# Kernel tuning notes

Measured on AMD Instinct MI355X. Metric: run time of the kernel, lower is better.

Reference implementation:

```python
import jax, jax.numpy as jnp
import numpy as np

B, T, I, H, FUT = 16384, 50, 6, 128, 30


def setup_inputs() -> dict:
    key = jax.random.key(0)
    ks = jax.random.split(key, 10)
    bound = 1.0 / np.sqrt(H)
    u = lambda k, shape: jax.random.uniform(k, shape, jnp.float32, -bound, bound)
    return {
        "history": jax.random.normal(ks[0], (B, T, I), jnp.float32),
        # GRU weights (PyTorch layout: gates stacked [r, z, n])
        "w_ih": u(ks[1], (3 * H, I)),
        "w_hh": u(ks[2], (3 * H, H)),
        "b_ih": u(ks[3], (3 * H,)),
        "b_hh": u(ks[4], (3 * H,)),
        # MLP head: Linear(H,H) -> ReLU -> Linear(H,I)
        "w1": u(ks[5], (H, H)),
        "b1": u(ks[6], (H,)),
        "w2": u(ks[7], (I, H)),
        "b2": u(ks[8], (I,)),
    }


def _gru_cell(h, x, w_ih, w_hh, b_ih, b_hh):
    # PyTorch GRU cell: gates ordered r, z, n
    gi = x @ w_ih.T + b_ih          # (B, 3H)
    gh = h @ w_hh.T + b_hh          # (B, 3H)
    i_r, i_z, i_n = jnp.split(gi, 3, axis=-1)
    h_r, h_z, h_n = jnp.split(gh, 3, axis=-1)
    r = jax.nn.sigmoid(i_r + h_r)
    z = jax.nn.sigmoid(i_z + h_z)
    n = jnp.tanh(i_n + r * h_n)
    return (1.0 - z) * n + z * h


def reference(history, w_ih, w_hh, b_ih, b_hh, w1, b1, w2, b2):
    # --- encode history: scan GRU over time ---
    h0 = jnp.zeros((history.shape[0], H), history.dtype)

    def enc_step(h, x_t):
        return _gru_cell(h, x_t, w_ih, w_hh, b_ih, b_hh), None

    h_last, _ = jax.lax.scan(enc_step, h0, jnp.swapaxes(history, 0, 1))  # (B, H)

    def head(h):
        return jax.nn.relu(h @ w1.T + b1) @ w2.T + b2  # (B, I)

    def dec_step(carry, _):
        h, x = carry
        h = _gru_cell(h, x, w_ih, w_hh, b_ih, b_hh)
        x = head(h)
        return (h, x), x

    x0 = history[:, -1]  # (B, I)
    _, preds = jax.lax.scan(dec_step, (h_last, x0), None, length=FUT)  # (FUT, B, I)
    return jnp.swapaxes(preds, 0, 1)  # (B, FUT, I)
```

## Files before the change

### kernel.cpp

```cpp
#include <hip/hip_runtime.h>

typedef _Float16 half8 __attribute__((ext_vector_type(8)));
typedef _Float16 half4 __attribute__((ext_vector_type(4)));
typedef float f32x4 __attribute__((ext_vector_type(4)));

#define ROWS 64
#define HP 136
#define HBUFSZ (ROWS * HP)
#define LOG2E 1.442695041f
#define MFMA(a,b,c) __builtin_amdgcn_mfma_f32_16x16x32_f16((a),(b),(c),0,0,0)

__global__ __launch_bounds__(512, 2)
void traj_gru(const float* __restrict__ history,
              const float* __restrict__ w_ih, const float* __restrict__ w_hh,
              const float* __restrict__ b_ih, const float* __restrict__ b_hh,
              const float* __restrict__ w1, const float* __restrict__ b1,
              const float* __restrict__ w2, const float* __restrict__ b2,
              float* __restrict__ out)
{
    __shared__ __align__(16) _Float16 hbuf[2 * HBUFSZ];
    __shared__ __align__(16) _Float16 xhist[50 * ROWS * 8];
    __shared__ __align__(16) _Float16 xdec[ROWS * 8];
    __shared__ __align__(16) _Float16 w2f[4 * 4 * 16 * 8];

    const int tid  = threadIdx.x;
    const int wave = tid >> 6;
    const int lane = tid & 63;
    const int ln16 = lane & 15;
    const int q    = lane >> 4;
    const int sw   = ln16 & 3;
    const int rowbase = blockIdx.x * ROWS;
    const int dbase = wave * 16;
    const int bblk  = wave >> 1;
    const int colin = ((wave & 1) << 4) | ln16;

    for (int i = tid; i < 2 * HBUFSZ; i += 512) hbuf[i] = (_Float16)0;
    for (int i = tid; i < ROWS * 8; i += 512) xdec[i] = (_Float16)0;
    for (int i = tid; i < 4 * 4 * 16 * 8; i += 512) w2f[i] = (_Float16)0;
    __syncthreads();
    for (int idx = tid; idx < 50 * ROWS * 8; idx += 512) {
        int c = idx & 7, tr = idx >> 3;
        int r = tr & (ROWS - 1), t = tr >> 6;
        _Float16 v;
        if (c < 6)       v = (_Float16)history[(rowbase + r) * 300 + t * 6 + c];
        else if (c == 6) v = (_Float16)1.0f;
        else             v = (_Float16)0.0f;
        xhist[idx] = v;
    }
    if (tid < ROWS) xdec[tid * 8 + 6] = (_Float16)1.0f;
    for (int idx = tid; idx < 6 * 128; idx += 512) {
        int n = idx >> 7, k = idx & 127;
        int kt = k >> 5, qq = (k >> 3) & 3, j = k & 7;
        w2f[((kt * 4 + qq) * 16 + n) * 8 + j] = (_Float16)w2[n * 128 + k];
    }

    half8 Wg[3][4];
    #pragma unroll
    for (int g = 0; g < 3; ++g) {
        float sc = (g < 2) ? -LOG2E : -2.0f * LOG2E;
        #pragma unroll
        for (int kt = 0; kt < 4; ++kt) {
            const float* p = w_hh + (g * 128 + dbase + ln16) * 128 + kt * 32 + q * 8;
            half8 v;
            #pragma unroll
            for (int j = 0; j < 8; ++j) v[j] = (_Float16)(p[j] * sc);
            Wg[g][kt] = v;
        }
    }
    half8 Wx[3];
    #pragma unroll
    for (int g = 0; g < 3; ++g) {
        float sc = (g < 2) ? -LOG2E : -2.0f * LOG2E;
        half8 v;
        #pragma unroll
        for (int j = 0; j < 8; ++j) v[j] = (_Float16)0.0f;
        if (q == 0) {
            #pragma unroll
            for (int j = 0; j < 6; ++j) v[j] = (_Float16)(w_ih[(g * 128 + dbase + ln16) * 6 + j] * sc);
        }
        Wx[g] = v;
    }
    f32x4 brr, brz, bin, bhn;
    #pragma unroll
    for (int i = 0; i < 4; ++i) {
        int d = dbase + q * 4 + i;
        brr[i] = (b_ih[d]       + b_hh[d]      ) * (-LOG2E);
        brz[i] = (b_ih[128 + d] + b_hh[128 + d]) * (-LOG2E);
        bin[i] = b_ih[256 + d] * (-2.0f * LOG2E);
        bhn[i] = b_hh[256 + d] * (-2.0f * LOG2E);
    }
    half8 Bw1[4];
    #pragma unroll
    for (int kt = 0; kt < 4; ++kt) {
        const float* p = w1 + (dbase + ln16) * 128 + kt * 32 + q * 8;
        half8 v;
        #pragma unroll
        for (int j = 0; j < 8; ++j) v[j] = (_Float16)p[j];
        Bw1[kt] = v;
    }
    const float b1r = b1[dbase + ln16];
    const float b2r = (ln16 < 6) ? b2[ln16] : 0.0f;

    float hp[4][4] = {};

    __syncthreads();

    auto gru_step = [&](int p, int t, bool enc) {
        const _Float16* hb = hbuf + p * HBUFSZ;
        _Float16*       hn = hbuf + (p ^ 1) * HBUFSZ;
        half8 Bf[2][4], Bx[2];
        f32x4 ar[2], az[2], ahh[2], an[2];

        auto loadB = [&](int c, int buf) {
            const _Float16* rp = hb + (c * 16 + ln16) * HP;
            #pragma unroll
            for (int kt = 0; kt < 4; ++kt)
                Bf[buf][kt] = *(const half8*)(rp + kt * 32 + q * 8);
            if (enc) {
                Bx[buf] = *(const half8*)(xhist + ((t * ROWS + c * 16 + ln16) << 3));
            } else {
                Bx[buf] = *(const half8*)(xdec + (c * 16 + ln16) * 8);
            }
        };
        auto mfmas = [&](int buf) {
            f32x4 r = brr, z = brz, hh = bhn, n = bin;
            __builtin_amdgcn_s_setprio(1);
            #pragma unroll
            for (int kt = 0; kt < 4; ++kt) {
                r  = MFMA(Wg[0][kt], Bf[buf][kt], r);
                z  = MFMA(Wg[1][kt], Bf[buf][kt], z);
                hh = MFMA(Wg[2][kt], Bf[buf][kt], hh);
            }
            r = MFMA(Wx[0], Bx[buf], r);
            z = MFMA(Wx[1], Bx[buf], z);
            n = MFMA(Wx[2], Bx[buf], n);
            __builtin_amdgcn_s_setprio(0);
            ar[buf] = r; az[buf] = z; ahh[buf] = hh; an[buf] = n;
        };
        auto gates = [&](int c, int cb) {
            half4 hv;
            #pragma unroll
            for (int i = 0; i < 4; ++i) {
                float r = __builtin_amdgcn_rcpf(1.0f + __builtin_amdgcn_exp2f(ar[cb][i]));
                float z = __builtin_amdgcn_rcpf(1.0f + __builtin_amdgcn_exp2f(az[cb][i]));
                float tt = an[cb][i] + r * ahh[cb][i];
                float n = 2.0f * __builtin_amdgcn_rcpf(1.0f + __builtin_amdgcn_exp2f(tt)) - 1.0f;
                float h = n + z * (hp[c][i] - n);
                hp[c][i] = h;
                hv[i] = (_Float16)h;
            }
            *(half4*)(hn + (c * 16 + ln16) * HP + dbase + q * 4) = hv;
        };

        loadB(0, 0); mfmas(0);
        #pragma unroll
        for (int c = 0; c < 4; ++c) {
            const int cb = c & 1;
            if (c < 3) { loadB(c + 1, cb ^ 1); mfmas(cb ^ 1); }
            gates(c, cb);
        }
        __syncthreads();
    };

    auto head_step = [&](int f, int p) {
        const _Float16* hb = hbuf + p * HBUFSZ;
        _Float16*       a1 = hbuf + (p ^ 1) * HBUFSZ;
        half8 Ah[2][4];
        f32x4 aa[2];
        auto loadA = [&](int c, int buf) {
            const _Float16* rp = hb + (c * 16 + ln16) * HP;
            #pragma unroll
            for (int kt = 0; kt < 4; ++kt)
                Ah[buf][kt] = *(const half8*)(rp + kt * 32 + q * 8);
        };
        auto mfh = [&](int buf) {
            f32x4 a = {0,0,0,0};
            __builtin_amdgcn_s_setprio(1);
            #pragma unroll
            for (int kt = 0; kt < 4; ++kt) a = MFMA(Ah[buf][kt], Bw1[kt], a);
            __builtin_amdgcn_s_setprio(0);
            aa[buf] = a;
        };
        auto relu4 = [&](int c, int cb) {
            #pragma unroll
            for (int i = 0; i < 4; ++i) {
                float v = aa[cb][i] + b1r;
                v = v > 0.0f ? v : 0.0f;
                a1[(c * 16 + q * 4 + i) * HP + ((bblk ^ i) << 5) + colin] = (_Float16)v;
            }
        };
        loadA(0, 0); mfh(0);
        #pragma unroll
        for (int c = 0; c < 4; ++c) {
            const int cb = c & 1;
            if (c < 3) { loadA(c + 1, cb ^ 1); mfh(cb ^ 1); }
            relu4(c, cb);
        }
        __syncthreads();
        if (wave < 4) {
            const _Float16* rp = a1 + (wave * 16 + ln16) * HP;
            f32x4 o = {0,0,0,0};
            #pragma unroll
            for (int kt = 0; kt < 4; ++kt) {
                half8 Aa = *(const half8*)(rp + ((kt ^ sw) << 5) + q * 8);
                half8 Bw = *(const half8*)&w2f[((kt * 4 + q) * 16 + ln16) * 8];
                o = MFMA(Aa, Bw, o);
            }
            if (ln16 < 6) {
                #pragma unroll
                for (int i = 0; i < 4; ++i) {
                    int row = wave * 16 + q * 4 + i;
                    float v = o[i] + b2r;
                    out[(rowbase + row) * 180 + f * 6 + ln16] = v;
                    xdec[row * 8 + ln16] = (_Float16)v;
                }
            }
        }
        __syncthreads();
    };

    int p = 0;
    #pragma unroll 1
    for (int t = 0; t < 50; ++t) { gru_step(p, t, true); p ^= 1; }
    #pragma unroll 1
    for (int f = 0; f < 30; ++f) {
        gru_step(p, f == 0 ? 49 : 0, f == 0);
        p ^= 1;
        head_step(f, p);
    }
}

extern "C" void kernel_launch(void* const* d_in, const int* in_sizes, int n_in,
                              void* d_out, int out_size, void* d_ws, size_t ws_size,
                              hipStream_t stream) {
    (void)in_sizes; (void)n_in; (void)d_ws; (void)ws_size; (void)out_size;
    traj_gru<<<dim3(16384 / ROWS), dim3(512), 0, stream>>>(
        (const float*)d_in[0], (const float*)d_in[1], (const float*)d_in[2],
        (const float*)d_in[3], (const float*)d_in[4], (const float*)d_in[5],
        (const float*)d_in[6], (const float*)d_in[7], (const float*)d_in[8],
        (float*)d_out);
}
```

Before: 288.2 us.

## Software-pipeline encoder GRU steps across time with split-half barriers

Replaces the encoder loop with a dedicated pipelined loop. The four 16-row chunks are split into two halves with a barrier between them, so the next timestep's MFMAs for the first half can run while the gate math for the second half of the current step finishes. The aim is to hide the dependency stall between the MFMA results and the transcendental gate work. It costs a second barrier per step and more live accumulator registers, which may reduce occupancy. The setprio hints are also removed from the decoder MFMA blocks.

```diff
diff --git a/kernel.cpp b/kernel.cpp
--- a/kernel.cpp
+++ b/kernel.cpp
@@ -105,6 +105,62 @@
 
     __syncthreads();
 
+    {
+        f32x4 aA[2][4], aB[2][4];
+        auto emfma = [&](int t, int c, f32x4 (&acc)[4]) {
+            const _Float16* rp = hbuf + (t & 1) * HBUFSZ + (c * 16 + ln16) * HP;
+            half8 b0 = *(const half8*)(rp +  0 + q * 8);
+            half8 b1v = *(const half8*)(rp + 32 + q * 8);
+            half8 b2v = *(const half8*)(rp + 64 + q * 8);
+            half8 b3 = *(const half8*)(rp + 96 + q * 8);
+            half8 bx = *(const half8*)(xhist + ((t * ROWS + c * 16 + ln16) << 3));
+            f32x4 r = brr, z = brz, hh = bhn, n = bin;
+            r = MFMA(Wg[0][0], b0, r);  z = MFMA(Wg[1][0], b0, z);  hh = MFMA(Wg[2][0], b0, hh);
+            r = MFMA(Wg[0][1], b1v, r); z = MFMA(Wg[1][1], b1v, z); hh = MFMA(Wg[2][1], b1v, hh);
+            r = MFMA(Wg[0][2], b2v, r); z = MFMA(Wg[1][2], b2v, z); hh = MFMA(Wg[2][2], b2v, hh);
+            r = MFMA(Wg[0][3], b3, r);  z = MFMA(Wg[1][3], b3, z);  hh = MFMA(Wg[2][3], b3, hh);
+            r = MFMA(Wx[0], bx, r);
+            z = MFMA(Wx[1], bx, z);
+            n = MFMA(Wx[2], bx, n);
+            acc[0] = r; acc[1] = z; acc[2] = hh; acc[3] = n;
+        };
+        auto egates = [&](int t, int c, f32x4 (&acc)[4]) {
+            _Float16* hn = hbuf + ((t & 1) ^ 1) * HBUFSZ;
+            half4 hv;
+            #pragma unroll
+            for (int i = 0; i < 4; ++i) {
+                float rr = __builtin_amdgcn_rcpf(1.0f + __builtin_amdgcn_exp2f(acc[0][i]));
+                float zz = __builtin_amdgcn_rcpf(1.0f + __builtin_amdgcn_exp2f(acc[1][i]));
+                float tt = acc[3][i] + rr * acc[2][i];
+                float nn = 2.0f * __builtin_amdgcn_rcpf(1.0f + __builtin_amdgcn_exp2f(tt)) - 1.0f;
+                float h = nn + zz * (hp[c][i] - nn);
+                hp[c][i] = h;
+                hv[i] = (_Float16)h;
+            }
+            *(half4*)(hn + (c * 16 + ln16) * HP + dbase + q * 4) = hv;
+        };
+
+        emfma(0, 0, aA[0]); emfma(0, 1, aA[1]);
+        #pragma unroll 1
+        for (int t = 0; t < 50; ++t) {
+            emfma(t, 2, aB[0]);
+            egates(t, 0, aA[0]);
+            emfma(t, 3, aB[1]);
+            egates(t, 1, aA[1]);
+            __syncthreads();
+            if (t < 49) {
+                emfma(t + 1, 0, aA[0]);
+                egates(t, 2, aB[0]);
+                emfma(t + 1, 1, aA[1]);
+                egates(t, 3, aB[1]);
+                __syncthreads();
+            }
+        }
+        egates(49, 2, aB[0]);
+        egates(49, 3, aB[1]);
+        __syncthreads();
+    }
+
     auto gru_step = [&](int p, int t, bool enc) {
         const _Float16* hb = hbuf + p * HBUFSZ;
         _Float16*       hn = hbuf + (p ^ 1) * HBUFSZ;
@@ -124,7 +180,6 @@
         };
         auto mfmas = [&](int buf) {
             f32x4 r = brr, z = brz, hh = bhn, n = bin;
-            __builtin_amdgcn_s_setprio(1);
             #pragma unroll
             for (int kt = 0; kt < 4; ++kt) {
                 r  = MFMA(Wg[0][kt], Bf[buf][kt], r);
@@ -134,7 +189,6 @@
             r = MFMA(Wx[0], Bx[buf], r);
             z = MFMA(Wx[1], Bx[buf], z);
             n = MFMA(Wx[2], Bx[buf], n);
-            __builtin_amdgcn_s_setprio(0);
             ar[buf] = r; az[buf] = z; ahh[buf] = hh; an[buf] = n;
         };
         auto gates = [&](int c, int cb) {
@@ -175,10 +229,8 @@
         };
         auto mfh = [&](int buf) {
             f32x4 a = {0,0,0,0};
-            __builtin_amdgcn_s_setprio(1);
             #pragma unroll
             for (int kt = 0; kt < 4; ++kt) a = MFMA(Ah[buf][kt], Bw1[kt], a);
-            __builtin_amdgcn_s_setprio(0);
             aa[buf] = a;
         };
         auto relu4 = [&](int c, int cb) {
@@ -220,8 +272,6 @@
     };
 
     int p = 0;
-    #pragma unroll 1
-    for (int t = 0; t < 50; ++t) { gru_step(p, t, true); p ^= 1; }
     #pragma unroll 1
     for (int f = 0; f < 30; ++f) {
         gru_step(p, f == 0 ? 49 : 0, f == 0);
```

Measured after the change: 288.9 us. No clear change (+0.2%).
